# Performance work log

Hardware: AMD Instinct MI355X
Metric: run time of the kernel (lower is better)

Reference implementation:

```python
import jax, jax.numpy as jnp
import numpy as np

N_NODES = 1_000_000
N_EDGES = 5_000_000


def setup_inputs() -> dict:
    key = jax.random.key(0)
    k1, k2, k3, k4 = jax.random.split(key, 4)
    x = jax.random.normal(k1, (N_NODES, 1), dtype=jnp.float32)
    edge_index = jax.random.randint(k2, (2, N_EDGES), 0, N_NODES, dtype=jnp.int64)
    # GCNConv params: lin weight (in,out) applied before propagation, bias after.
    W1 = jax.random.normal(k3, (1, 16), dtype=jnp.float32) / jnp.sqrt(1.0)
    b1 = jnp.zeros((16,), dtype=jnp.float32)
    W2 = jax.random.normal(k4, (16, 1), dtype=jnp.float32) / jnp.sqrt(16.0)
    b2 = jnp.zeros((1,), dtype=jnp.float32)
    return {"x": x, "edge_index": edge_index, "W1": W1, "b1": b1, "W2": W2, "b2": b2}


def _gcn_conv(x, W, b, src, dst, n_nodes):
    """GCNConv: out = D^{-1/2} (A + I) D^{-1/2} (x W) + b."""
    h = x @ W  # [N, F_out]
    loops = jnp.arange(n_nodes, dtype=src.dtype)
    s = jnp.concatenate([src, loops])  # [E+N]
    d = jnp.concatenate([dst, loops])
    # degree from destination index (edge weights = 1), incl. self loops
    deg = jax.ops.segment_sum(jnp.ones_like(d, dtype=h.dtype), d, num_segments=n_nodes)
    dinv = jnp.where(deg > 0, jax.lax.rsqrt(deg), 0.0)
    norm = dinv[s] * dinv[d]  # [E+N]
    msg = h[s] * norm[:, None]  # gather + scale, [E+N, F_out]
    out = jax.ops.segment_sum(msg, d, num_segments=n_nodes)  # scatter-add
    return out + b


def reference(x, edge_index, W1, b1, W2, b2):
    src, dst = edge_index[0], edge_index[1]
    n = x.shape[0]
    h = jax.nn.relu(_gcn_conv(x, W1, b1, src, dst, n))
    return _gcn_conv(h, W2, b2, src, dst, n)
```

## Files before the change

kernel.cpp:

```cpp
#include <hip/hip_runtime.h>
#include <hip/hip_cooperative_groups.h>

namespace cg = cooperative_groups;

#define THREADS 256
#define BSH 11
#define BSZ 2048
#define NBMAX 512
#define ST 8192
#define SCT 512
#define EPT 16
#define BT 1024
#define LDSE 12800
#define SMASK 0xFFFFFu


__global__ void k_init(unsigned* __restrict__ gcur, unsigned C, int NB) {
    int t = threadIdx.x;
    if (t < NB) gcur[t] = (unsigned)t * C;
}

__global__ void __launch_bounds__(SCT)
k_scatter(const int* __restrict__ src,
          const int* __restrict__ dst, int E,
          unsigned* __restrict__ gcur,
          unsigned* __restrict__ packed, unsigned C, int NB) {
    __shared__ unsigned tcnt[NBMAX];
    __shared__ unsigned toff[NBMAX];
    __shared__ unsigned gb[NBMAX];
    __shared__ unsigned sh[NBMAX];
    __shared__ unsigned sorted[ST];
    __shared__ unsigned short jarr[ST];

    int tid = threadIdx.x;
    int lo = blockIdx.x * ST;
    int cnt = E - lo; if (cnt > ST) cnt = ST;

    tcnt[tid] = 0u;
    __syncthreads();

    unsigned jreg[EPT], rreg[EPT], rank[EPT];
    #pragma unroll
    for (int kk = 0; kk < EPT / 4; ++kk) {
        int g = kk * SCT + tid;
        int base = g * 4;
        if (base + 3 < cnt) {
            int4 d4 = *(const int4*)(dst + lo + base);
            int4 s4 = *(const int4*)(src + lo + base);
            unsigned j0 = (unsigned)d4.x >> BSH;
            unsigned j1 = (unsigned)d4.y >> BSH;
            unsigned j2 = (unsigned)d4.z >> BSH;
            unsigned j3 = (unsigned)d4.w >> BSH;
            jreg[kk*4+0] = j0; rreg[kk*4+0] = (unsigned)s4.x | (((unsigned)d4.x & (BSZ-1)) << 20);
            jreg[kk*4+1] = j1; rreg[kk*4+1] = (unsigned)s4.y | (((unsigned)d4.y & (BSZ-1)) << 20);
            jreg[kk*4+2] = j2; rreg[kk*4+2] = (unsigned)s4.z | (((unsigned)d4.z & (BSZ-1)) << 20);
            jreg[kk*4+3] = j3; rreg[kk*4+3] = (unsigned)s4.w | (((unsigned)d4.w & (BSZ-1)) << 20);
            rank[kk*4+0] = atomicAdd(&tcnt[j0], 1u);
            rank[kk*4+1] = atomicAdd(&tcnt[j1], 1u);
            rank[kk*4+2] = atomicAdd(&tcnt[j2], 1u);
            rank[kk*4+3] = atomicAdd(&tcnt[j3], 1u);
        } else {
            #pragma unroll
            for (int c = 0; c < 4; ++c) {
                int idx = base + c;
                if (idx < cnt) {
                    int d = dst[lo + idx];
                    unsigned jj = (unsigned)d >> BSH;
                    jreg[kk*4+c] = jj;
                    rreg[kk*4+c] = (unsigned)src[lo + idx] | (((unsigned)d & (BSZ-1)) << 20);
                    rank[kk*4+c] = atomicAdd(&tcnt[jj], 1u);
                } else {
                    jreg[kk*4+c] = ~0u;
                }
            }
        }
    }
    __syncthreads();

    unsigned v = tcnt[tid];
    sh[tid] = v;
    __syncthreads();
    for (int off = 1; off < NBMAX; off <<= 1) {
        unsigned t = (tid >= off) ? sh[tid - off] : 0u;
        __syncthreads();
        sh[tid] += t;
        __syncthreads();
    }
    {
        unsigned excl = sh[tid] - v;
        toff[tid] = excl;
        if (v) gb[tid] = atomicAdd(&gcur[tid], v);
    }
    __syncthreads();

    #pragma unroll
    for (int k = 0; k < EPT; ++k) {
        unsigned jj = jreg[k];
        if (jj != ~0u) {
            unsigned p = toff[jj] + rank[k];
            sorted[p] = rreg[k];
            jarr[p] = (unsigned short)jj;
        }
    }
    __syncthreads();

    for (int p = tid; p < cnt; p += SCT) {
        unsigned jj = jarr[p];
        unsigned pos = gb[jj] + ((unsigned)p - toff[jj]);
        if (pos < (jj + 1u) * C) packed[pos] = sorted[p];
    }
}

__global__ void __launch_bounds__(BT, 8)
k_fused(const unsigned* __restrict__ packed,
        const unsigned* __restrict__ gcur, unsigned C,
        const float* __restrict__ x,
        const float* __restrict__ W1, const float* __restrict__ b1,
        const float* __restrict__ W2, const float* __restrict__ b2,
        float* __restrict__ dinv, float* __restrict__ y,
        float* __restrict__ zy, float* __restrict__ out,
        int N, int F) {
    cg::grid_group grid = cg::this_grid();
    __shared__ __align__(16) unsigned recs[LDSE];
    __shared__ unsigned cntl[BSZ];
    __shared__ float    accf[BSZ];
    __shared__ float    w1s[64], b1s[64], w2s[64];

    const int j = blockIdx.x;
    const unsigned tid = threadIdx.x;
    const int base = j << BSH;

    for (int t = tid; t < BSZ; t += BT) cntl[t] = 0u;
    if (tid < (unsigned)F) {
        w1s[tid] = W1[tid]; b1s[tid] = b1[tid]; w2s[tid] = W2[tid];
    }
    __syncthreads();

    unsigned e0 = (unsigned)j * C;
    unsigned e1 = gcur[j]; if (e1 > e0 + C) e1 = e0 + C;
    const unsigned n = e1 - e0;
    const unsigned nv4 = n >> 2;

    for (unsigned g = tid; g < nv4; g += BT) {
        uint4 a = *(const uint4*)(packed + e0 + (size_t)g * 4u);
        ((uint4*)recs)[g] = a;
        atomicAdd(&cntl[a.x >> 20], 1u);
        atomicAdd(&cntl[a.y >> 20], 1u);
        atomicAdd(&cntl[a.z >> 20], 1u);
        atomicAdd(&cntl[a.w >> 20], 1u);
    }
    for (unsigned e = nv4 * 4u + tid; e < n; e += BT) {
        unsigned p = packed[e0 + e];
        recs[e] = p;
        atomicAdd(&cntl[p >> 20], 1u);
    }
    __syncthreads();
    for (int t = tid; t < BSZ; t += BT) {
        int v = base + t;
        if (v < N) {
            float d = rsqrtf((float)cntl[t] + 1.0f);
            dinv[v] = d;
            y[v] = x[v] * d;
        }
    }
    grid.sync();

    for (int t = tid; t < BSZ; t += BT) accf[t] = 0.f;
    __syncthreads();
    {
        unsigned i = tid;
        for (; i + 3u * BT < n; i += 4u * BT) {
            unsigned p0 = recs[i],          p1 = recs[i + BT];
            unsigned p2 = recs[i + 2u*BT],  p3 = recs[i + 3u*BT];
            float v0 = y[p0 & SMASK], v1 = y[p1 & SMASK];
            float v2 = y[p2 & SMASK], v3 = y[p3 & SMASK];
            atomicAdd(&accf[p0 >> 20], v0);
            atomicAdd(&accf[p1 >> 20], v1);
            atomicAdd(&accf[p2 >> 20], v2);
            atomicAdd(&accf[p3 >> 20], v3);
        }
        for (; i < n; i += BT) {
            unsigned p = recs[i];
            atomicAdd(&accf[p >> 20], y[p & SMASK]);
        }
    }
    __syncthreads();
    for (int t = tid; t < BSZ; t += BT) {
        int v = base + t;
        if (v < N) {
            float d = dinv[v];
            float agg = d * (accf[t] + y[v]);
            float z = 0.f;
            for (int f = 0; f < F; ++f) {
                float h = fmaf(w1s[f], agg, b1s[f]);
                h = fmaxf(h, 0.f);
                z = fmaf(h, w2s[f], z);
            }
            zy[v] = z * d;
        }
    }
    grid.sync();

    for (int t = tid; t < BSZ; t += BT) accf[t] = 0.f;
    __syncthreads();
    {
        unsigned i = tid;
        for (; i + 3u * BT < n; i += 4u * BT) {
            unsigned p0 = recs[i],          p1 = recs[i + BT];
            unsigned p2 = recs[i + 2u*BT],  p3 = recs[i + 3u*BT];
            float v0 = zy[p0 & SMASK], v1 = zy[p1 & SMASK];
            float v2 = zy[p2 & SMASK], v3 = zy[p3 & SMASK];
            atomicAdd(&accf[p0 >> 20], v0);
            atomicAdd(&accf[p1 >> 20], v1);
            atomicAdd(&accf[p2 >> 20], v2);
            atomicAdd(&accf[p3 >> 20], v3);
        }
        for (; i < n; i += BT) {
            unsigned p = recs[i];
            atomicAdd(&accf[p >> 20], zy[p & SMASK]);
        }
    }
    __syncthreads();
    for (int t = tid; t < BSZ; t += BT) {
        int v = base + t;
        if (v < N)
            out[v] = fmaf(dinv[v], accf[t] + zy[v], b2[0]);
    }
}


__global__ void k_deg(const unsigned* __restrict__ packed,
                      const unsigned* __restrict__ gcur, unsigned C,
                      const float* __restrict__ x,
                      float* __restrict__ dinv, float* __restrict__ y, int N) {
    int j = blockIdx.x;
    __shared__ unsigned cntl[BSZ];
    for (int t = threadIdx.x; t < BSZ; t += BT) cntl[t] = 0u;
    __syncthreads();
    unsigned e0 = (unsigned)j * C;
    unsigned e1 = gcur[j]; if (e1 > e0 + C) e1 = e0 + C;
    unsigned tid = threadIdx.x;
    unsigned nv4 = (e1 - e0) >> 2;
    for (unsigned g = tid; g < nv4; g += BT) {
        uint4 a = *(const uint4*)(packed + e0 + (size_t)g * 4u);
        atomicAdd(&cntl[a.x >> 20], 1u);
        atomicAdd(&cntl[a.y >> 20], 1u);
        atomicAdd(&cntl[a.z >> 20], 1u);
        atomicAdd(&cntl[a.w >> 20], 1u);
    }
    for (unsigned e = e0 + nv4 * 4u + tid; e < e1; e += BT)
        atomicAdd(&cntl[packed[e] >> 20], 1u);
    __syncthreads();
    int base = j << BSH;
    for (int t = threadIdx.x; t < BSZ; t += BT) {
        int v = base + t;
        if (v < N) {
            float d = rsqrtf((float)cntl[t] + 1.0f);
            dinv[v] = d;
            y[v] = x[v] * d;
        }
    }
}

__global__ void k_acc1(const unsigned* __restrict__ packed,
                       const unsigned* __restrict__ gcur, unsigned C,
                       const float* __restrict__ y,
                       const float* __restrict__ dinv,
                       const float* __restrict__ W1,
                       const float* __restrict__ b1,
                       const float* __restrict__ W2,
                       float* __restrict__ zy, int N, int F) {
    int j = blockIdx.x;
    __shared__ float acc[BSZ];
    __shared__ float w1s[64], b1s[64], w2s[64];
    for (int t = threadIdx.x; t < BSZ; t += BT) acc[t] = 0.f;
    if (threadIdx.x < (unsigned)F) {
        w1s[threadIdx.x] = W1[threadIdx.x];
        b1s[threadIdx.x] = b1[threadIdx.x];
        w2s[threadIdx.x] = W2[threadIdx.x];
    }
    __syncthreads();
    unsigned e0 = (unsigned)j * C;
    unsigned e1 = gcur[j]; if (e1 > e0 + C) e1 = e0 + C;
    unsigned tid = threadIdx.x;
    unsigned nv4 = (e1 - e0) >> 2;
    for (unsigned g = tid; g < nv4; g += BT) {
        uint4 a = *(const uint4*)(packed + e0 + (size_t)g * 4u);
        float v0 = y[a.x & SMASK], v1 = y[a.y & SMASK];
        float v2 = y[a.z & SMASK], v3 = y[a.w & SMASK];
        atomicAdd(&acc[a.x >> 20], v0);
        atomicAdd(&acc[a.y >> 20], v1);
        atomicAdd(&acc[a.z >> 20], v2);
        atomicAdd(&acc[a.w >> 20], v3);
    }
    for (unsigned e = e0 + nv4 * 4u + tid; e < e1; e += BT) {
        unsigned p = packed[e];
        atomicAdd(&acc[p >> 20], y[p & SMASK]);
    }
    __syncthreads();
    int base = j << BSH;
    for (int t = threadIdx.x; t < BSZ; t += BT) {
        int v = base + t;
        if (v < N) {
            float d = dinv[v];
            float agg = d * (acc[t] + y[v]);
            float z = 0.f;
            for (int f = 0; f < F; ++f) {
                float h = fmaf(w1s[f], agg, b1s[f]);
                h = fmaxf(h, 0.f);
                z = fmaf(h, w2s[f], z);
            }
            zy[v] = z * d;
        }
    }
}

__global__ void k_out(const unsigned* __restrict__ packed,
                      const unsigned* __restrict__ gcur, unsigned C,
                      const float* __restrict__ zy,
                      const float* __restrict__ dinv,
                      const float* __restrict__ b2,
                      float* __restrict__ out, int N) {
    int j = blockIdx.x;
    __shared__ float acc[BSZ];
    for (int t = threadIdx.x; t < BSZ; t += BT) acc[t] = 0.f;
    __syncthreads();
    unsigned e0 = (unsigned)j * C;
    unsigned e1 = gcur[j]; if (e1 > e0 + C) e1 = e0 + C;
    unsigned tid = threadIdx.x;
    unsigned nv4 = (e1 - e0) >> 2;
    for (unsigned g = tid; g < nv4; g += BT) {
        uint4 a = *(const uint4*)(packed + e0 + (size_t)g * 4u);
        float v0 = zy[a.x & SMASK], v1 = zy[a.y & SMASK];
        float v2 = zy[a.z & SMASK], v3 = zy[a.w & SMASK];
        atomicAdd(&acc[a.x >> 20], v0);
        atomicAdd(&acc[a.y >> 20], v1);
        atomicAdd(&acc[a.z >> 20], v2);
        atomicAdd(&acc[a.w >> 20], v3);
    }
    for (unsigned e = e0 + nv4 * 4u + tid; e < e1; e += BT) {
        unsigned p = packed[e];
        atomicAdd(&acc[p >> 20], zy[p & SMASK]);
    }
    __syncthreads();
    int base = j << BSH;
    for (int t = threadIdx.x; t < BSZ; t += BT) {
        int v = base + t;
        if (v < N)
            out[v] = fmaf(dinv[v], acc[t] + zy[v], b2[0]);
    }
}


__global__ void f_zero3(float* __restrict__ a, float* __restrict__ b,
                        float* __restrict__ c, int N) {
    int i = blockIdx.x * blockDim.x + threadIdx.x;
    int stride = gridDim.x * blockDim.x;
    for (int v = i; v < N; v += stride) { a[v] = 0.f; b[v] = 0.f; c[v] = 0.f; }
}
__global__ void f_deg(const int* __restrict__ dst, int E, float* __restrict__ degf) {
    int i = blockIdx.x * blockDim.x + threadIdx.x;
    int stride = gridDim.x * blockDim.x;
    for (int e = i; e < E; e += stride) atomicAdd(&degf[dst[e]], 1.0f);
}
__global__ void f_dinv(float* __restrict__ d, int N) {
    int v = blockIdx.x * blockDim.x + threadIdx.x;
    if (v < N) d[v] = rsqrtf(d[v] + 1.0f);
}
__global__ void f_edge1(const int* __restrict__ src, const int* __restrict__ dst,
                        const float* __restrict__ x, const float* __restrict__ dinv,
                        float* __restrict__ acc1, int E) {
    int i = blockIdx.x * blockDim.x + threadIdx.x;
    int stride = gridDim.x * blockDim.x;
    for (int e = i; e < E; e += stride) {
        int s = src[e];
        atomicAdd(&acc1[dst[e]], x[s] * dinv[s]);
    }
}
__global__ void f_node2(const float* __restrict__ dinv, const float* __restrict__ acc1,
                        const float* __restrict__ x, const float* __restrict__ W1,
                        const float* __restrict__ b1, const float* __restrict__ W2,
                        float* __restrict__ zy, int N, int F) {
    int v = blockIdx.x * blockDim.x + threadIdx.x;
    if (v < N) {
        float d = dinv[v];
        float agg = d * (acc1[v] + x[v] * d);
        float z = 0.f;
        for (int f = 0; f < F; ++f) {
            float h = fmaf(W1[f], agg, b1[f]);
            h = h > 0.f ? h : 0.f;
            z = fmaf(h, W2[f], z);
        }
        zy[v] = z * d;
    }
}
__global__ void f_edge2(const int* __restrict__ src, const int* __restrict__ dst,
                        const float* __restrict__ zy, float* __restrict__ out, int E) {
    int i = blockIdx.x * blockDim.x + threadIdx.x;
    int stride = gridDim.x * blockDim.x;
    for (int e = i; e < E; e += stride) atomicAdd(&out[dst[e]], zy[src[e]]);
}
__global__ void f_node3(const float* __restrict__ dinv, const float* __restrict__ zy,
                        const float* __restrict__ b2, float* __restrict__ out, int N) {
    int v = blockIdx.x * blockDim.x + threadIdx.x;
    if (v < N) out[v] = fmaf(dinv[v], out[v] + zy[v], b2[0]);
}


extern "C" void kernel_launch(void* const* d_in, const int* in_sizes, int n_in,
                              void* d_out, int out_size, void* d_ws, size_t ws_size,
                              hipStream_t stream) {
    const float* x  = (const float*)d_in[0];
    const int*   ei = (const int*)d_in[1];
    const float* W1 = (const float*)d_in[2];
    const float* b1 = (const float*)d_in[3];
    const float* W2 = (const float*)d_in[4];
    const float* b2 = (const float*)d_in[5];
    float* out = (float*)d_out;

    const int N = in_sizes[0];
    const int E = in_sizes[1] / 2;
    const int F = in_sizes[2];

    const int* src = ei;
    const int* dst = ei + E;

    const int NB = (N + BSZ - 1) >> BSH;

    unsigned mean = (unsigned)(E / (NB > 0 ? NB : 1));
    unsigned C = (mean + mean / 8u + 1024u + 3u) & ~3u;

    size_t off_packed = 0;
    size_t off_gc     = (off_packed + (size_t)NB * C * 4 + 15) & ~(size_t)15;
    size_t off_dinv   = (off_gc + (size_t)NBMAX * 4 + 15) & ~(size_t)15;
    size_t off_y      = off_dinv + (size_t)N * 4;
    size_t off_zy     = off_y + (size_t)N * 4;
    size_t need       = off_zy + (size_t)N * 4;

    bool ok = (ws_size >= need) && (NB >= 1) && (NB <= NBMAX) &&
              (N <= (1 << 20)) && (F <= 64) && (E > 0);

    char* ws = (char*)d_ws;
    if (ok) {
        unsigned* packed = (unsigned*)(ws + off_packed);
        unsigned* gcur   = (unsigned*)(ws + off_gc);
        float*    dinv   = (float*)(ws + off_dinv);
        float*    y      = (float*)(ws + off_y);
        float*    zy     = (float*)(ws + off_zy);

        int scatBlocks = (E + ST - 1) / ST;

        k_init   <<<1, NBMAX, 0, stream>>>(gcur, C, NB);
        k_scatter<<<scatBlocks, SCT, 0, stream>>>(src, dst, E, gcur, packed, C, NB);

        bool coop = (C <= LDSE);
        int occ = 0, cus = 0;
        if (coop) {
            if (hipOccupancyMaxActiveBlocksPerMultiprocessor(&occ, k_fused, BT, 0)
                    != hipSuccess) coop = false;
            int dev = 0;
            hipGetDevice(&dev);
            if (hipDeviceGetAttribute(&cus, hipDeviceAttributeMultiprocessorCount,
                                      dev) != hipSuccess) coop = false;
            if (coop && (long long)occ * cus < NB) coop = false;
        }
        if (coop) {
            unsigned Cv = C; int Nv = N, Fv = F;
            void* args[] = { (void*)&packed, (void*)&gcur, (void*)&Cv,
                             (void*)&x, (void*)&W1, (void*)&b1, (void*)&W2,
                             (void*)&b2, (void*)&dinv, (void*)&y, (void*)&zy,
                             (void*)&out, (void*)&Nv, (void*)&Fv };
            if (hipLaunchCooperativeKernel((const void*)k_fused, dim3(NB),
                                           dim3(BT), args, 0, stream)
                    != hipSuccess) coop = false;
        }
        if (!coop) {
            k_deg  <<<NB, BT, 0, stream>>>(packed, gcur, C, x, dinv, y, N);
            k_acc1 <<<NB, BT, 0, stream>>>(packed, gcur, C, y, dinv, W1, b1, W2, zy, N, F);
            k_out  <<<NB, BT, 0, stream>>>(packed, gcur, C, zy, dinv, b2, out, N);
        }
    } else {
        float* dinv = (float*)(ws);
        float* acc1 = (float*)(ws + (size_t)N * 4);
        float* zy   = (float*)(ws + (size_t)N * 8);
        int nodeBlocks = (N + THREADS - 1) / THREADS;
        int edgeBlocks = (E + THREADS - 1) / THREADS;
        if (edgeBlocks > 2048) edgeBlocks = 2048;
        f_zero3<<<2048, THREADS, 0, stream>>>(dinv, acc1, out, N);
        f_deg  <<<edgeBlocks, THREADS, 0, stream>>>(dst, E, dinv);
        f_dinv <<<nodeBlocks, THREADS, 0, stream>>>(dinv, N);
        f_edge1<<<edgeBlocks, THREADS, 0, stream>>>(src, dst, x, dinv, acc1, E);
        f_node2<<<nodeBlocks, THREADS, 0, stream>>>(dinv, acc1, x, W1, b1, W2, zy, N, F);
        f_edge2<<<edgeBlocks, THREADS, 0, stream>>>(src, dst, zy, out, E);
        f_node3<<<nodeBlocks, THREADS, 0, stream>>>(dinv, zy, b2, out, N);
    }
}
```

Measured before the change: 108.1 us.

## Replace cooperative fused kernel with per-block CSR build and atomic-free row gathers

Removes the cooperative grid-synced fused kernel and instead builds a per-bucket CSR (counting sort by local destination with a block-wide scan) in a separate kernel that also computes dinv and y. The two aggregation passes then walk each node's row serially, with no LDS atomics. This targets the LDS atomic contention and grid-sync cost of the old design. In exchange it adds an extra global CSR array write and reread, and row lengths vary per thread, so the gather loops can be imbalanced and poorly coalesced.

```diff
diff --git a/kernel.cpp b/kernel.cpp
--- a/kernel.cpp
+++ b/kernel.cpp
@@ -1,7 +1,4 @@
 #include <hip/hip_runtime.h>
-#include <hip/hip_cooperative_groups.h>
-
-namespace cg = cooperative_groups;
 
 #define THREADS 256
 #define BSH 11
@@ -11,7 +8,7 @@
 #define SCT 512
 #define EPT 16
 #define BT 1024
-#define LDSE 12800
+#define CEPT 16
 #define SMASK 0xFFFFFu
 
 
@@ -111,85 +108,130 @@
     }
 }
 
-__global__ void __launch_bounds__(BT, 8)
-k_fused(const unsigned* __restrict__ packed,
-        const unsigned* __restrict__ gcur, unsigned C,
-        const float* __restrict__ x,
-        const float* __restrict__ W1, const float* __restrict__ b1,
-        const float* __restrict__ W2, const float* __restrict__ b2,
-        float* __restrict__ dinv, float* __restrict__ y,
-        float* __restrict__ zy, float* __restrict__ out,
-        int N, int F) {
-    cg::grid_group grid = cg::this_grid();
-    __shared__ __align__(16) unsigned recs[LDSE];
-    __shared__ unsigned cntl[BSZ];
-    __shared__ float    accf[BSZ];
-    __shared__ float    w1s[64], b1s[64], w2s[64];
-
-    const int j = blockIdx.x;
-    const unsigned tid = threadIdx.x;
-    const int base = j << BSH;
-
-    for (int t = tid; t < BSZ; t += BT) cntl[t] = 0u;
-    if (tid < (unsigned)F) {
-        w1s[tid] = W1[tid]; b1s[tid] = b1[tid]; w2s[tid] = W2[tid];
-    }
+__global__ void __launch_bounds__(BT)
+k_csr(const unsigned* __restrict__ packed,
+      const unsigned* __restrict__ gcur, unsigned C,
+      const float* __restrict__ x,
+      unsigned* __restrict__ csr, unsigned* __restrict__ rowptr,
+      float* __restrict__ dinv, float* __restrict__ y, int N) {
+    int j = blockIdx.x;
+    __shared__ unsigned cnt[BSZ];
+    __shared__ unsigned excl[BSZ];
+    __shared__ unsigned wsum[16];
+    unsigned tid = threadIdx.x;
+
+    for (int t = tid; t < BSZ; t += BT) cnt[t] = 0u;
     __syncthreads();
 
     unsigned e0 = (unsigned)j * C;
     unsigned e1 = gcur[j]; if (e1 > e0 + C) e1 = e0 + C;
     const unsigned n = e1 - e0;
-    const unsigned nv4 = n >> 2;
-
-    for (unsigned g = tid; g < nv4; g += BT) {
-        uint4 a = *(const uint4*)(packed + e0 + (size_t)g * 4u);
-        ((uint4*)recs)[g] = a;
-        atomicAdd(&cntl[a.x >> 20], 1u);
-        atomicAdd(&cntl[a.y >> 20], 1u);
-        atomicAdd(&cntl[a.z >> 20], 1u);
-        atomicAdd(&cntl[a.w >> 20], 1u);
-    }
-    for (unsigned e = nv4 * 4u + tid; e < n; e += BT) {
-        unsigned p = packed[e0 + e];
-        recs[e] = p;
-        atomicAdd(&cntl[p >> 20], 1u);
-    }
-    __syncthreads();
+
+    unsigned dl[CEPT], sr[CEPT], rk[CEPT];
+    #pragma unroll
+    for (int kk = 0; kk < CEPT / 4; ++kk) {
+        unsigned b4 = ((unsigned)kk * BT + tid) * 4u;
+        if (b4 + 3u < n) {
+            uint4 a = *(const uint4*)(packed + e0 + (size_t)b4);
+            dl[kk*4+0] = a.x >> 20; sr[kk*4+0] = a.x & SMASK;
+            dl[kk*4+1] = a.y >> 20; sr[kk*4+1] = a.y & SMASK;
+            dl[kk*4+2] = a.z >> 20; sr[kk*4+2] = a.z & SMASK;
+            dl[kk*4+3] = a.w >> 20; sr[kk*4+3] = a.w & SMASK;
+            rk[kk*4+0] = atomicAdd(&cnt[dl[kk*4+0]], 1u);
+            rk[kk*4+1] = atomicAdd(&cnt[dl[kk*4+1]], 1u);
+            rk[kk*4+2] = atomicAdd(&cnt[dl[kk*4+2]], 1u);
+            rk[kk*4+3] = atomicAdd(&cnt[dl[kk*4+3]], 1u);
+        } else {
+            #pragma unroll
+            for (int c = 0; c < 4; ++c) {
+                unsigned idx = b4 + c;
+                if (idx < n) {
+                    unsigned p = packed[e0 + idx];
+                    dl[kk*4+c] = p >> 20; sr[kk*4+c] = p & SMASK;
+                    rk[kk*4+c] = atomicAdd(&cnt[p >> 20], 1u);
+                } else {
+                    dl[kk*4+c] = ~0u;
+                }
+            }
+        }
+    }
+    __syncthreads();
+
+    {
+        unsigned s0 = cnt[2u*tid], s1 = cnt[2u*tid + 1u];
+        unsigned T = s0 + s1;
+        unsigned incl = T;
+        #pragma unroll
+        for (int off = 1; off < 64; off <<= 1) {
+            unsigned u = __shfl_up(incl, off, 64);
+            if ((tid & 63u) >= (unsigned)off) incl += u;
+        }
+        unsigned wid = tid >> 6;
+        if ((tid & 63u) == 63u) wsum[wid] = incl;
+        __syncthreads();
+        if (tid < 16u) {
+            unsigned w = wsum[tid];
+            unsigned wi = w;
+            #pragma unroll
+            for (int off = 1; off < 16; off <<= 1) {
+                unsigned u = __shfl_up(wi, off, 64);
+                if (tid >= (unsigned)off) wi += u;
+            }
+            wsum[tid] = wi;
+        }
+        __syncthreads();
+        unsigned wbase = (wid == 0u) ? 0u : wsum[wid - 1u];
+        unsigned te = wbase + incl - T;
+        excl[2u*tid] = te;
+        excl[2u*tid + 1u] = te + s0;
+    }
+    __syncthreads();
+
+    #pragma unroll
+    for (int k = 0; k < CEPT; ++k) {
+        if (dl[k] != ~0u) csr[e0 + excl[dl[k]] + rk[k]] = sr[k];
+    }
+
+    int base = j << BSH;
     for (int t = tid; t < BSZ; t += BT) {
         int v = base + t;
         if (v < N) {
-            float d = rsqrtf((float)cntl[t] + 1.0f);
+            float d = rsqrtf((float)cnt[t] + 1.0f);
             dinv[v] = d;
             y[v] = x[v] * d;
-        }
-    }
-    grid.sync();
-
-    for (int t = tid; t < BSZ; t += BT) accf[t] = 0.f;
-    __syncthreads();
-    {
-        unsigned i = tid;
-        for (; i + 3u * BT < n; i += 4u * BT) {
-            unsigned p0 = recs[i],          p1 = recs[i + BT];
-            unsigned p2 = recs[i + 2u*BT],  p3 = recs[i + 3u*BT];
-            float v0 = y[p0 & SMASK], v1 = y[p1 & SMASK];
-            float v2 = y[p2 & SMASK], v3 = y[p3 & SMASK];
-            atomicAdd(&accf[p0 >> 20], v0);
-            atomicAdd(&accf[p1 >> 20], v1);
-            atomicAdd(&accf[p2 >> 20], v2);
-            atomicAdd(&accf[p3 >> 20], v3);
-        }
-        for (; i < n; i += BT) {
-            unsigned p = recs[i];
-            atomicAdd(&accf[p >> 20], y[p & SMASK]);
-        }
-    }
-    __syncthreads();
-    for (int t = tid; t < BSZ; t += BT) {
+            rowptr[v] = e0 + excl[t];
+        }
+    }
+}
+
+__global__ void __launch_bounds__(BT)
+k2_acc1(const unsigned* __restrict__ csr,
+        const unsigned* __restrict__ gcur, unsigned C,
+        const unsigned* __restrict__ rowptr,
+        const float* __restrict__ y, const float* __restrict__ dinv,
+        const float* __restrict__ W1, const float* __restrict__ b1,
+        const float* __restrict__ W2,
+        float* __restrict__ zy, int N, int F) {
+    int j = blockIdx.x;
+    __shared__ float w1s[64], b1s[64], w2s[64];
+    if (threadIdx.x < (unsigned)F) {
+        w1s[threadIdx.x] = W1[threadIdx.x];
+        b1s[threadIdx.x] = b1[threadIdx.x];
+        w2s[threadIdx.x] = W2[threadIdx.x];
+    }
+    __syncthreads();
+    unsigned e0 = (unsigned)j * C;
+    unsigned e1 = gcur[j]; if (e1 > e0 + C) e1 = e0 + C;
+    int base = j << BSH;
+    for (int t = threadIdx.x; t < BSZ; t += BT) {
         int v = base + t;
         if (v < N) {
+            unsigned lo = rowptr[v];
+            unsigned hi = (t == BSZ - 1 || v + 1 >= N) ? e1 : rowptr[v + 1];
+            float s = 0.f;
+            for (unsigned e = lo; e < hi; ++e) s += y[csr[e]];
             float d = dinv[v];
-            float agg = d * (accf[t] + y[v]);
+            float agg = d * (s + y[v]);
             float z = 0.f;
             for (int f = 0; f < F; ++f) {
                 float h = fmaf(w1s[f], agg, b1s[f]);
@@ -199,32 +241,29 @@
             zy[v] = z * d;
         }
     }
-    grid.sync();
-
-    for (int t = tid; t < BSZ; t += BT) accf[t] = 0.f;
-    __syncthreads();
-    {
-        unsigned i = tid;
-        for (; i + 3u * BT < n; i += 4u * BT) {
-            unsigned p0 = recs[i],          p1 = recs[i + BT];
-            unsigned p2 = recs[i + 2u*BT],  p3 = recs[i + 3u*BT];
-            float v0 = zy[p0 & SMASK], v1 = zy[p1 & SMASK];
-            float v2 = zy[p2 & SMASK], v3 = zy[p3 & SMASK];
-            atomicAdd(&accf[p0 >> 20], v0);
-            atomicAdd(&accf[p1 >> 20], v1);
-            atomicAdd(&accf[p2 >> 20], v2);
-            atomicAdd(&accf[p3 >> 20], v3);
-        }
-        for (; i < n; i += BT) {
-            unsigned p = recs[i];
-            atomicAdd(&accf[p >> 20], zy[p & SMASK]);
-        }
-    }
-    __syncthreads();
-    for (int t = tid; t < BSZ; t += BT) {
+}
+
+__global__ void __launch_bounds__(BT)
+k2_out(const unsigned* __restrict__ csr,
+       const unsigned* __restrict__ gcur, unsigned C,
+       const unsigned* __restrict__ rowptr,
+       const float* __restrict__ zy, const float* __restrict__ dinv,
+       const float* __restrict__ b2,
+       float* __restrict__ out, int N) {
+    int j = blockIdx.x;
+    unsigned e0 = (unsigned)j * C;
+    unsigned e1 = gcur[j]; if (e1 > e0 + C) e1 = e0 + C;
+    int base = j << BSH;
+    float bb = b2[0];
+    for (int t = threadIdx.x; t < BSZ; t += BT) {
         int v = base + t;
-        if (v < N)
-            out[v] = fmaf(dinv[v], accf[t] + zy[v], b2[0]);
+        if (v < N) {
+            unsigned lo = rowptr[v];
+            unsigned hi = (t == BSZ - 1 || v + 1 >= N) ? e1 : rowptr[v + 1];
+            float s = 0.f;
+            for (unsigned e = lo; e < hi; ++e) s += zy[csr[e]];
+            out[v] = fmaf(dinv[v], s + zy[v], bb);
+        }
     }
 }
 
@@ -431,8 +470,10 @@
     unsigned C = (mean + mean / 8u + 1024u + 3u) & ~3u;
 
     size_t off_packed = 0;
-    size_t off_gc     = (off_packed + (size_t)NB * C * 4 + 15) & ~(size_t)15;
-    size_t off_dinv   = (off_gc + (size_t)NBMAX * 4 + 15) & ~(size_t)15;
+    size_t off_csr    = (off_packed + (size_t)NB * C * 4 + 15) & ~(size_t)15;
+    size_t off_gc     = (off_csr + (size_t)NB * C * 4 + 15) & ~(size_t)15;
+    size_t off_rp     = (off_gc + (size_t)NBMAX * 4 + 15) & ~(size_t)15;
+    size_t off_dinv   = off_rp + (size_t)N * 4;
     size_t off_y      = off_dinv + (size_t)N * 4;
     size_t off_zy     = off_y + (size_t)N * 4;
     size_t need       = off_zy + (size_t)N * 4;
@@ -443,7 +484,9 @@
     char* ws = (char*)d_ws;
     if (ok) {
         unsigned* packed = (unsigned*)(ws + off_packed);
+        unsigned* csr    = (unsigned*)(ws + off_csr);
         unsigned* gcur   = (unsigned*)(ws + off_gc);
+        unsigned* rowptr = (unsigned*)(ws + off_rp);
         float*    dinv   = (float*)(ws + off_dinv);
         float*    y      = (float*)(ws + off_y);
         float*    zy     = (float*)(ws + off_zy);
@@ -453,28 +496,11 @@
         k_init   <<<1, NBMAX, 0, stream>>>(gcur, C, NB);
         k_scatter<<<scatBlocks, SCT, 0, stream>>>(src, dst, E, gcur, packed, C, NB);
 
-        bool coop = (C <= LDSE);
-        int occ = 0, cus = 0;
-        if (coop) {
-            if (hipOccupancyMaxActiveBlocksPerMultiprocessor(&occ, k_fused, BT, 0)
-                    != hipSuccess) coop = false;
-            int dev = 0;
-            hipGetDevice(&dev);
-            if (hipDeviceGetAttribute(&cus, hipDeviceAttributeMultiprocessorCount,
-                                      dev) != hipSuccess) coop = false;
-            if (coop && (long long)occ * cus < NB) coop = false;
-        }
-        if (coop) {
-            unsigned Cv = C; int Nv = N, Fv = F;
-            void* args[] = { (void*)&packed, (void*)&gcur, (void*)&Cv,
-                             (void*)&x, (void*)&W1, (void*)&b1, (void*)&W2,
-                             (void*)&b2, (void*)&dinv, (void*)&y, (void*)&zy,
-                             (void*)&out, (void*)&Nv, (void*)&Fv };
-            if (hipLaunchCooperativeKernel((const void*)k_fused, dim3(NB),
-                                           dim3(BT), args, 0, stream)
-                    != hipSuccess) coop = false;
-        }
-        if (!coop) {
+        if (C <= (unsigned)(CEPT * BT)) {
+            k_csr  <<<NB, BT, 0, stream>>>(packed, gcur, C, x, csr, rowptr, dinv, y, N);
+            k2_acc1<<<NB, BT, 0, stream>>>(csr, gcur, C, rowptr, y, dinv, W1, b1, W2, zy, N, F);
+            k2_out <<<NB, BT, 0, stream>>>(csr, gcur, C, rowptr, zy, dinv, b2, out, N);
+        } else {
             k_deg  <<<NB, BT, 0, stream>>>(packed, gcur, C, x, dinv, y, N);
             k_acc1 <<<NB, BT, 0, stream>>>(packed, gcur, C, y, dinv, W1, b1, W2, zy, N, F);
             k_out  <<<NB, BT, 0, stream>>>(packed, gcur, C, zy, dinv, b2, out, N);
```

Measured after the change: 154.3 us. 42.7% more time.
